# Optimization experiments

Hardware: AMD Instinct MI355X
Metric: run time of the kernel (lower is better)

Reference implementation:

```python
import jax, jax.numpy as jnp
import numpy as np

NUM_USERS = 100000
NUM_ITEMS = 50000
NUM_HIDDEN = 64
NUM_BINS = 10
BATCH = 131072
N_QUAD = 64  # quadrature nodes in incomplete/complete beta
EPS = 1e-6


def _trapz0(y, dt):
    # trapezoidal rule along axis 0 with uniform spacing dt
    return (jnp.sum(y, axis=0) - 0.5 * (y[0] + y[-1])) * dt


def setup_inputs() -> dict:
    key = jax.random.key(0)
    ks = jax.random.split(key, 12)
    return {
        "uid_input": jax.random.randint(ks[0], (BATCH,), 0, NUM_USERS),
        "iid_input": jax.random.randint(ks[1], (BATCH,), 0, NUM_ITEMS),
        "uid_features": 0.1 * jax.random.normal(ks[2], (NUM_USERS, NUM_HIDDEN + 1), jnp.float32),
        "iid_features": 0.1 * jax.random.normal(ks[3], (NUM_ITEMS, NUM_HIDDEN + 1), jnp.float32),
        "uid_bin_terms": 0.1 * jax.random.normal(ks[4], (NUM_USERS, NUM_BINS), jnp.float32),
        "iid_bin_terms": 0.1 * jax.random.normal(ks[5], (NUM_ITEMS, NUM_BINS), jnp.float32),
        "uid_alpha_emb": 0.01 * jax.random.normal(ks[6], (NUM_USERS, 1), jnp.float32),
        "uid_beta_emb": 0.01 * jax.random.normal(ks[7], (NUM_USERS, 1), jnp.float32),
        "iid_alpha_emb": 0.01 * jax.random.normal(ks[8], (NUM_ITEMS, 1), jnp.float32),
        "iid_beta_emb": 0.01 * jax.random.normal(ks[9], (NUM_ITEMS, 1), jnp.float32),
        "global_bias": jnp.asarray(2.0, jnp.float32),
    }


def reference(uid_input, iid_input, uid_features, iid_features,
              uid_bin_terms, iid_bin_terms, uid_alpha_emb, uid_beta_emb,
              iid_alpha_emb, iid_beta_emb, global_bias):
    # embedding lookups (confidence features alias the regular features)
    uf = uid_features[uid_input]          # (B, H+1)
    vf = iid_features[iid_input]          # (B, H+1)
    u = uf[:, :-1]                        # (B, H)
    v = vf[:, :-1]

    # mu / upsilon (upsilon_layer_id == 2: |dot|)
    dot = jnp.sum(u * v, axis=-1, keepdims=True)                    # (B, 1)
    len_prod = (jnp.linalg.norm(u, axis=1, keepdims=True)
                * jnp.linalg.norm(v, axis=1, keepdims=True))
    mu = jnp.clip(0.5 + 0.5 * dot / jnp.maximum(len_prod, EPS), EPS, 1.0 - EPS)
    upsilon = jnp.maximum(jnp.abs(dot), EPS)

    # alpha / beta
    alpha = jnp.maximum(0.01, mu * upsilon)
    beta = jnp.maximum(0.01, upsilon - alpha)
    alpha = global_bias + alpha
    beta = global_bias + beta
    alpha = jnp.maximum(0.01, alpha + uid_alpha_emb[uid_input] + iid_alpha_emb[iid_input])  # (B,1)
    beta = jnp.maximum(0.01, beta + uid_beta_emb[uid_input] + iid_beta_emb[iid_input])      # (B,1)

    # per-pair bin edges via normalized exp + cumsum
    terms = jnp.exp(uid_bin_terms[uid_input] + iid_bin_terms[iid_input])  # (B, NUM_BINS)
    terms = terms / jnp.sum(terms, axis=-1, keepdims=True)
    edges = jnp.cumsum(terms, axis=-1)                                    # (B, NUM_BINS)

    # regularized incomplete beta at interior edges via trapezoidal quadrature
    x = edges[:, :-1]                                  # (B, NB-1)
    t = jnp.linspace(0.0, 1.0, N_QUAD, dtype=alpha.dtype)
    dt = t[1] - t[0]
    t3 = t[:, None, None]                              # (n, 1, 1)
    a3 = alpha[None, :, :]                             # (1, B, 1)
    b3 = beta[None, :, :]
    tx = t3 * x[None]                                  # (n, B, NB-1)
    integrand = (tx ** (a3 - 1.0)) * ((1.0 - tx) ** (b3 - 1.0))
    integrand = integrand * (t3 <= x[None]).astype(integrand.dtype)
    Bx_ab = _trapz0(integrand, dt)                     # (B, NB-1)

    # complete beta B(a, b)
    c_int = (t[None, :] ** (alpha - 1.0)) * ((1.0 - t[None, :]) ** (beta - 1.0))  # (B, n)
    B_ab = (jnp.sum(c_int, axis=-1) - 0.5 * (c_int[:, 0] + c_int[:, -1])) * dt    # (B,)

    cdf = Bx_ab / B_ab[:, None]                        # (B, NB-1)
    cdf = jnp.concatenate([cdf, jnp.ones_like(alpha)], axis=-1)  # (B, NB)
    mass = jnp.concatenate([cdf[:, :1], cdf[:, 1:] - cdf[:, :-1]], axis=-1)
    return mass
```

## Files before the change

### kernel.cpp

```cpp
#include <hip/hip_runtime.h>
#include <math.h>

#define BLOCK 256
#define SPB (BLOCK / 4)

struct F4a4 { float a, b, c, d; };

__device__ __forceinline__ float exp2_fast(float x) {
#if __has_builtin(__builtin_amdgcn_exp2f)
    return __builtin_amdgcn_exp2f(x);
#else
    return __expf(x * 0.69314718055994531f);
#endif
}

__device__ __forceinline__ double exp_f64_fast(double x) {
    const double L2E = 1.4426950408889634074;
    const double LN2 = 0.69314718055994530942;
    double n = rint(x * L2E);
    double r = fma(x, L2E, -n);
    double w = r * LN2;
    double p = 2.08767569878680989792e-9;
    p = fma(p, w, 2.50521083854417187751e-8);
    p = fma(p, w, 2.75573192239858906526e-7);
    p = fma(p, w, 2.75573192239858925110e-6);
    p = fma(p, w, 2.48015873015873015873e-5);
    p = fma(p, w, 1.98412698412698412698e-4);
    p = fma(p, w, 1.38888888888888888889e-3);
    p = fma(p, w, 8.33333333333333333333e-3);
    p = fma(p, w, 4.16666666666666666667e-2);
    p = fma(p, w, 1.66666666666666666667e-1);
    p = fma(p, w, 0.5);
    p = fma(p, w, 1.0);
    p = fma(p, w, 1.0);
    const double sc = __longlong_as_double((long long)(1023 + (int)n) << 52);
    return p * sc;
}

__global__ __launch_bounds__(BLOCK) void lbd_kernel(
    const int* __restrict__ uid_in, const int* __restrict__ iid_in,
    const float* __restrict__ uf,  const float* __restrict__ vf,
    const float* __restrict__ ubt, const float* __restrict__ ibt,
    const float* __restrict__ uae, const float* __restrict__ ube,
    const float* __restrict__ iae, const float* __restrict__ ibe,
    const float* __restrict__ gbp, float* __restrict__ out, int B)
{
    __shared__ float2 s_num[72];
    __shared__ float2 s_den[64];
    const int tid = threadIdx.x;
    if (tid < 72) {
        const double STEP0 = 1.0 / 63.0;
        float tf = (tid >= 63) ? 1.0f : (float)((double)tid * STEP0);
        const float lt = __log2f(tf);
        s_num[tid] = make_float2(tf, lt);
        if (tid < 64) s_den[tid] = make_float2(lt, __log2f(1.0f - tf));
    }
    __syncthreads();

    const int sub = tid & 3;
    const int s0  = blockIdx.x * SPB + (tid >> 2);
    const bool valid = (s0 < B);
    const int s = valid ? s0 : (B - 1);

    const int u = uid_in[s];
    const int v = iid_in[s];

    const float* pu = uf + (long long)u * 65;
    const float* pv = vf + (long long)v * 65;
    float dotp = 0.f, sup = 0.f, svp = 0.f;
#pragma unroll
    for (int c = 0; c < 4; ++c) {
        const F4a4 a = *(const F4a4*)(pu + c * 16 + sub * 4);
        const F4a4 b = *(const F4a4*)(pv + c * 16 + sub * 4);
        dotp += a.a * b.a + a.b * b.b + a.c * b.c + a.d * b.d;
        sup  += a.a * a.a + a.b * a.b + a.c * a.c + a.d * a.d;
        svp  += b.a * b.a + b.b * b.b + b.c * b.c + b.d * b.d;
    }
#pragma unroll
    for (int d = 1; d < 4; d <<= 1) {
        dotp += __shfl_xor(dotp, d, 64);
        sup  += __shfl_xor(sup,  d, 64);
        svp  += __shfl_xor(svp,  d, 64);
    }

    float emb;
    {
        const float* ep = (sub == 0) ? (uae + u)
                        : (sub == 1) ? (iae + v)
                        : (sub == 2) ? (ube + u)
                        :              (ibe + v);
        emb = *ep;
    }
    const float ua_ = __shfl(emb, 0, 4);
    const float ia_ = __shfl(emb, 1, 4);
    const float ub_ = __shfl(emb, 2, 4);
    const float ib_ = __shfl(emb, 3, 4);

    const float gb = gbp[0];
    const float len_prod = sqrtf(sup) * sqrtf(svp);
    const float EPS = 1e-6f;
    const float HI  = (float)(1.0 - 1e-6);
    float mu = 0.5f + (0.5f * dotp) / fmaxf(len_prod, EPS);
    mu = fminf(fmaxf(mu, EPS), HI);
    const float ups = fmaxf(fabsf(dotp), EPS);
    const float al0 = fmaxf(0.01f, mu * ups);
    const float be0 = fmaxf(0.01f, ups - al0);
    const float alpha = fmaxf(0.01f, ((gb + al0) + ua_) + ia_);
    const float beta  = fmaxf(0.01f, ((gb + be0) + ub_) + ib_);
    const float am1 = alpha - 1.0f;
    const float bm1 = beta  - 1.0f;

    const double STEP = 1.0 / 63.0;
    const int lb = 3 * sub;
    double e0, e1 = 0.0, e2 = 0.0;
    {
        const long long ur = (long long)u * 10, vr = (long long)v * 10;
        const int i1 = (lb + 1 <= 9) ? lb + 1 : 9;
        const int i2 = (lb + 2 <= 9) ? lb + 2 : 9;
        e0 = exp_f64_fast((double)ubt[ur + lb] + (double)ibt[vr + lb]);
        const double t1 = exp_f64_fast((double)ubt[ur + i1] + (double)ibt[vr + i1]);
        const double t2 = exp_f64_fast((double)ubt[ur + i2] + (double)ibt[vr + i2]);
        if (lb + 1 <= 9) e1 = t1;
        if (lb + 2 <= 9) e2 = t2;
    }
    const double c0 = e0, c1 = c0 + e1, c2 = c1 + e2;
    double p = c2;
#pragma unroll
    for (int d = 1; d < 4; d <<= 1) {
        const double t = __shfl_up(p, d, 4);
        if (sub >= d) p += t;
    }
    const double ssum = __shfl(p, 3, 4);
    const double rsum = 1.0 / ssum;
    const double ex   = p - c2;
    float xf_own[3] = {0.f, 0.f, 0.f}, lx_own[3] = {0.f, 0.f, 0.f};
    int   im_own[3] = {0, 0, 0};
    const double cg0 = ex + c0, cg1 = ex + c1, cg2 = ex + c2;
#pragma unroll
    for (int r = 0; r < 3; ++r) {
        const double cgr = (r == 0) ? cg0 : (r == 1) ? cg1 : cg2;
        if (lb + r <= 8) {
            const double x = cgr * rsum;
            int k = (int)(x * 63.0);
            k = (k > 62) ? 62 : k;
            const int dec = ((double)k * STEP > x) ? 1 : 0;
            const int inc = ((k < 62) && ((double)(k + 1) * STEP <= x)) ? 1 : 0;
            im_own[r] = k + inc - dec;
            xf_own[r] = (float)x;
            lx_own[r] = __log2f(xf_own[r]);
        }
    }

    float xfj[9], alxj[9];
    int   imj[9], Mw[9];
#pragma unroll
    for (int j = 0; j < 9; ++j) {
        const int src  = j / 3;
        const int slot = j % 3;
        const float xo = (slot == 0) ? xf_own[0] : (slot == 1) ? xf_own[1] : xf_own[2];
        const float lo = (slot == 0) ? lx_own[0] : (slot == 1) ? lx_own[1] : lx_own[2];
        const int   io = (slot == 0) ? im_own[0] : (slot == 1) ? im_own[1] : im_own[2];
        xfj[j]  = __shfl(xo, src, 4);
        alxj[j] = am1 * __shfl(lo, src, 4);
        imj[j]  = __shfl(io, src, 4);
        int mm = imj[j];
        mm = max(mm, __shfl_xor(mm, 4, 64));
        mm = max(mm, __shfl_xor(mm, 8, 64));
        mm = max(mm, __shfl_xor(mm, 16, 64));
        mm = max(mm, __shfl_xor(mm, 32, 64));
        Mw[j] = __builtin_amdgcn_readfirstlane((mm + 3) >> 2);
    }

    float accD = 0.f;
#pragma unroll
    for (int m = 0; m < 16; ++m) {
        const float2 dd = s_den[m * 4 + sub];
        accD += exp2_fast(fmaf(bm1, dd.y, am1 * dd.x));
    }

    const float2 P0 = s_num[sub + 1];
    const float2 P1 = s_num[sub + 5];

    float acc[9];

#define MERGED_LOOP(j1, j2)                                                        \
    {                                                                              \
        const float xA = xfj[j1], aA = alxj[j1];                                   \
        const float xB = xfj[j2], aB = alxj[j2];                                   \
        const int   iA = imj[j1], iB = imj[j2];                                    \
        const int   M  = (Mw[j1] > Mw[j2]) ? Mw[j1] : Mw[j2];          \
        float aA0 = 0.f, aA1 = 0.f, aB0 = 0.f, aB1 = 0.f;                          \
        float2 t0 = P0, t1 = P1;                                                   \
        int m = 0;                                                                 \
        for (; m + 2 <= M; m += 2) {                                               \
            const float2 n0 = s_num[(m + 2) * 4 + sub + 1];                        \
            const float2 n1 = s_num[(m + 3) * 4 + sub + 1];                        \
            const int i0 = m * 4 + sub + 1;                                        \
            const int i1 = i0 + 4;                                                 \
            const float wA0 = fmaf(-t0.x, xA, 1.0f);                               \
            const float wA1 = fmaf(-t1.x, xA, 1.0f);                               \
            const float wB0 = fmaf(-t0.x, xB, 1.0f);                               \
            const float wB1 = fmaf(-t1.x, xB, 1.0f);                               \
            const float eA0 = fmaf(bm1, __log2f(wA0), fmaf(am1, t0.y, aA));        \
            const float eA1 = fmaf(bm1, __log2f(wA1), fmaf(am1, t1.y, aA));        \
            const float eB0 = fmaf(bm1, __log2f(wB0), fmaf(am1, t0.y, aB));        \
            const float eB1 = fmaf(bm1, __log2f(wB1), fmaf(am1, t1.y, aB));        \
            const float yA0 = exp2_fast(eA0), yA1 = exp2_fast(eA1);                \
            const float yB0 = exp2_fast(eB0), yB1 = exp2_fast(eB1);                \
            aA0 += (i0 <= iA) ? yA0 : 0.f;                                         \
            aA1 += (i1 <= iA) ? yA1 : 0.f;                                         \
            aB0 += (i0 <= iB) ? yB0 : 0.f;                                         \
            aB1 += (i1 <= iB) ? yB1 : 0.f;                                         \
            t0 = n0; t1 = n1;                                                      \
        }                                                                          \
        if (m < M) {                                                               \
            const int i0 = m * 4 + sub + 1;                                        \
            const float wA0 = fmaf(-t0.x, xA, 1.0f);                               \
            const float wB0 = fmaf(-t0.x, xB, 1.0f);                               \
            const float eA0 = fmaf(bm1, __log2f(wA0), fmaf(am1, t0.y, aA));        \
            const float eB0 = fmaf(bm1, __log2f(wB0), fmaf(am1, t0.y, aB));        \
            aA0 += (i0 <= iA) ? exp2_fast(eA0) : 0.f;                              \
            aB0 += (i0 <= iB) ? exp2_fast(eB0) : 0.f;                              \
        }                                                                          \
        acc[j1] = aA0 + aA1;                                                       \
        acc[j2] = aB0 + aB1;                                                       \
    }

    MERGED_LOOP(0, 1)
    MERGED_LOOP(2, 3)
    MERGED_LOOP(4, 5)
    MERGED_LOOP(6, 7)
#undef MERGED_LOOP

    {
        const float xj  = xfj[8];
        const float axj = alxj[8];
        const int   imv = imj[8];
        const int   M   = Mw[8];
        float a0 = 0.f, a1 = 0.f;
        float2 t0 = P0, t1 = P1;
        int m = 0;
        for (; m + 2 <= M; m += 2) {
            const float2 n0 = s_num[(m + 2) * 4 + sub + 1];
            const float2 n1 = s_num[(m + 3) * 4 + sub + 1];
            const int i0 = m * 4 + sub + 1;
            const int i1 = i0 + 4;
            const float w0 = fmaf(-t0.x, xj, 1.0f);
            const float w1 = fmaf(-t1.x, xj, 1.0f);
            const float e0v = fmaf(bm1, __log2f(w0), fmaf(am1, t0.y, axj));
            const float e1v = fmaf(bm1, __log2f(w1), fmaf(am1, t1.y, axj));
            const float y0 = exp2_fast(e0v);
            const float y1 = exp2_fast(e1v);
            a0 += (i0 <= imv) ? y0 : 0.f;
            a1 += (i1 <= imv) ? y1 : 0.f;
            t0 = n0; t1 = n1;
        }
        if (m < M) {
            const int i0 = m * 4 + sub + 1;
            const float w0 = fmaf(-t0.x, xj, 1.0f);
            const float e0v = fmaf(bm1, __log2f(w0), fmaf(am1, t0.y, axj));
            a0 += (i0 <= imv) ? exp2_fast(e0v) : 0.f;
        }
        acc[8] = a0 + a1;
    }

#pragma unroll
    for (int d = 1; d < 4; d <<= 1) {
        accD += __shfl_xor(accD, d, 64);
#pragma unroll
        for (int j = 0; j < 9; ++j) acc[j] += __shfl_xor(acc[j], d, 64);
    }

    const float dtf = (float)(1.0 / 63.0);
    const float rB  = 1.0f / (accD * dtf);
    float cdfv[9];
#pragma unroll
    for (int j = 0; j < 9; ++j) cdfv[j] = (acc[j] * dtf) * rB;

    const float o0 = (sub == 0) ? cdfv[0]
                   : (sub == 1) ? (cdfv[1] - cdfv[0])
                   : (sub == 2) ? (cdfv[2] - cdfv[1])
                   :              (cdfv[3] - cdfv[2]);
    const float o1 = (sub == 0) ? (cdfv[4] - cdfv[3])
                   : (sub == 1) ? (cdfv[5] - cdfv[4])
                   : (sub == 2) ? (cdfv[6] - cdfv[5])
                   :              (cdfv[7] - cdfv[6]);
    const float o2 = (sub == 0) ? (cdfv[8] - cdfv[7])
                   :              (1.0f - cdfv[8]);
    if (valid) {
        const long long ob = (long long)s * 10;
        out[ob + sub]     = o0;
        out[ob + 4 + sub] = o1;
        if (sub < 2) out[ob + 8 + sub] = o2;
    }
}

extern "C" void kernel_launch(void* const* d_in, const int* in_sizes, int n_in,
                              void* d_out, int out_size, void* d_ws, size_t ws_size,
                              hipStream_t stream) {
    (void)n_in; (void)out_size; (void)d_ws; (void)ws_size;
    const int*   uid = (const int*)d_in[0];
    const int*   iid = (const int*)d_in[1];
    const float* uf  = (const float*)d_in[2];
    const float* vf  = (const float*)d_in[3];
    const float* ubt = (const float*)d_in[4];
    const float* ibt = (const float*)d_in[5];
    const float* uae = (const float*)d_in[6];
    const float* ube = (const float*)d_in[7];
    const float* iae = (const float*)d_in[8];
    const float* ibe = (const float*)d_in[9];
    const float* gb  = (const float*)d_in[10];
    float* out = (float*)d_out;
    const int B = in_sizes[0];
    const int grid = (B + SPB - 1) / SPB;
    hipLaunchKernelGGL(lbd_kernel, dim3(grid), dim3(BLOCK), 0, stream,
                       uid, iid, uf, vf, ubt, ibt, uae, ube, iae, ibe, gb, out, B);
}
```

Baseline: 124.3 us.

## Stage per-sample edge values in LDS and fuse complete-beta sum into last loop

Per-sample edge values (x, log2 x, index bound) are now written to shared memory and read back by every lane of the group, replacing the register shuffle redistribution. The per-pair wave-max bound is computed inside each pair loop. The complete-beta denominator accumulation is merged into the final edge's quadrature loop, which now runs the full 16 iterations instead of a data-dependent bound. The aim is fewer cross-lane shuffles and better interleaving of transcendental work, at the cost of extra LDS traffic, a block barrier, and always running the full range for the last edge.

```diff
diff --git a/kernel.cpp b/kernel.cpp
--- a/kernel.cpp
+++ b/kernel.cpp
@@ -45,20 +45,34 @@
     const float* __restrict__ iae, const float* __restrict__ ibe,
     const float* __restrict__ gbp, float* __restrict__ out, int B)
 {
-    __shared__ float2 s_num[72];
-    __shared__ float2 s_den[64];
+    __shared__ float2 s_num[76];
+    __shared__ float2 s_den[72];
+    __shared__ float  s_x [SPB][10];
+    __shared__ float  s_lx[SPB][10];
+    __shared__ int    s_im[SPB][10];
+
     const int tid = threadIdx.x;
-    if (tid < 72) {
+    {
         const double STEP0 = 1.0 / 63.0;
-        float tf = (tid >= 63) ? 1.0f : (float)((double)tid * STEP0);
-        const float lt = __log2f(tf);
-        s_num[tid] = make_float2(tf, lt);
-        if (tid < 64) s_den[tid] = make_float2(lt, __log2f(1.0f - tf));
+        if (tid < 76) {
+            const float tf = (tid >= 63) ? 1.0f : (float)((double)tid * STEP0);
+            s_num[tid] = make_float2(tf, __log2f(tf));
+        }
+        if (tid < 72) {
+            float l1 = 0.f, l2 = 0.f;
+            if (tid < 64) {
+                const float tf = (tid >= 63) ? 1.0f : (float)((double)tid * STEP0);
+                l1 = __log2f(tf);
+                l2 = __log2f(1.0f - tf);
+            }
+            s_den[tid] = make_float2(l1, l2);
+        }
     }
     __syncthreads();
 
     const int sub = tid & 3;
-    const int s0  = blockIdx.x * SPB + (tid >> 2);
+    const int g   = tid >> 2;
+    const int s0  = blockIdx.x * SPB + g;
     const bool valid = (s0 < B);
     const int s = valid ? s0 : (B - 1);
 
@@ -133,8 +147,6 @@
     const double ssum = __shfl(p, 3, 4);
     const double rsum = 1.0 / ssum;
     const double ex   = p - c2;
-    float xf_own[3] = {0.f, 0.f, 0.f}, lx_own[3] = {0.f, 0.f, 0.f};
-    int   im_own[3] = {0, 0, 0};
     const double cg0 = ex + c0, cg1 = ex + c1, cg2 = ex + c2;
 #pragma unroll
     for (int r = 0; r < 3; ++r) {
@@ -145,50 +157,31 @@
             k = (k > 62) ? 62 : k;
             const int dec = ((double)k * STEP > x) ? 1 : 0;
             const int inc = ((k < 62) && ((double)(k + 1) * STEP <= x)) ? 1 : 0;
-            im_own[r] = k + inc - dec;
-            xf_own[r] = (float)x;
-            lx_own[r] = __log2f(xf_own[r]);
+            const float xf = (float)x;
+            s_im[g][lb + r] = k + inc - dec;
+            s_x [g][lb + r] = xf;
+            s_lx[g][lb + r] = __log2f(xf);
         }
     }
-
-    float xfj[9], alxj[9];
-    int   imj[9], Mw[9];
-#pragma unroll
-    for (int j = 0; j < 9; ++j) {
-        const int src  = j / 3;
-        const int slot = j % 3;
-        const float xo = (slot == 0) ? xf_own[0] : (slot == 1) ? xf_own[1] : xf_own[2];
-        const float lo = (slot == 0) ? lx_own[0] : (slot == 1) ? lx_own[1] : lx_own[2];
-        const int   io = (slot == 0) ? im_own[0] : (slot == 1) ? im_own[1] : im_own[2];
-        xfj[j]  = __shfl(xo, src, 4);
-        alxj[j] = am1 * __shfl(lo, src, 4);
-        imj[j]  = __shfl(io, src, 4);
-        int mm = imj[j];
-        mm = max(mm, __shfl_xor(mm, 4, 64));
-        mm = max(mm, __shfl_xor(mm, 8, 64));
-        mm = max(mm, __shfl_xor(mm, 16, 64));
-        mm = max(mm, __shfl_xor(mm, 32, 64));
-        Mw[j] = __builtin_amdgcn_readfirstlane((mm + 3) >> 2);
-    }
-
-    float accD = 0.f;
-#pragma unroll
-    for (int m = 0; m < 16; ++m) {
-        const float2 dd = s_den[m * 4 + sub];
-        accD += exp2_fast(fmaf(bm1, dd.y, am1 * dd.x));
-    }
+    __syncthreads();
 
     const float2 P0 = s_num[sub + 1];
     const float2 P1 = s_num[sub + 5];
 
     float acc[9];
-
-#define MERGED_LOOP(j1, j2)                                                        \
+    float accD = 0.f;
+
+#define PAIR_LOOP(j1, j2)                                                          \
     {                                                                              \
-        const float xA = xfj[j1], aA = alxj[j1];                                   \
-        const float xB = xfj[j2], aB = alxj[j2];                                   \
-        const int   iA = imj[j1], iB = imj[j2];                                    \
-        const int   M  = (Mw[j1] > Mw[j2]) ? Mw[j1] : Mw[j2];          \
+        const float xA = s_x[g][j1],          xB = s_x[g][j2];                     \
+        const float aA = am1 * s_lx[g][j1],   aB = am1 * s_lx[g][j2];              \
+        const int   iA = s_im[g][j1],         iB = s_im[g][j2];                    \
+        int mm = (iA > iB) ? iA : iB;                                              \
+        mm = max(mm, __shfl_xor(mm, 4, 64));    \
+        mm = max(mm, __shfl_xor(mm, 8, 64));                                       \
+        mm = max(mm, __shfl_xor(mm, 16, 64));                                      \
+        mm = max(mm, __shfl_xor(mm, 32, 64));                                      \
+        const int M = __builtin_amdgcn_readfirstlane((mm + 3) >> 2);               \
         float aA0 = 0.f, aA1 = 0.f, aB0 = 0.f, aB1 = 0.f;                          \
         float2 t0 = P0, t1 = P1;                                                   \
         int m = 0;                                                                 \
@@ -226,23 +219,25 @@
         acc[j2] = aB0 + aB1;                                                       \
     }
 
-    MERGED_LOOP(0, 1)
-    MERGED_LOOP(2, 3)
-    MERGED_LOOP(4, 5)
-    MERGED_LOOP(6, 7)
-#undef MERGED_LOOP
+    PAIR_LOOP(0, 1)
+    PAIR_LOOP(2, 3)
+    PAIR_LOOP(4, 5)
+    PAIR_LOOP(6, 7)
+#undef PAIR_LOOP
 
     {
-        const float xj  = xfj[8];
-        const float axj = alxj[8];
-        const int   imv = imj[8];
-        const int   M   = Mw[8];
+        const float xj  = s_x[g][8];
+        const float axj = am1 * s_lx[g][8];
+        const int   imv = s_im[g][8];
         float a0 = 0.f, a1 = 0.f;
         float2 t0 = P0, t1 = P1;
-        int m = 0;
-        for (; m + 2 <= M; m += 2) {
-            const float2 n0 = s_num[(m + 2) * 4 + sub + 1];
-            const float2 n1 = s_num[(m + 3) * 4 + sub + 1];
+        float2 d0 = s_den[sub], d1 = s_den[sub + 4];
+#pragma unroll 4
+        for (int m = 0; m + 2 <= 16; m += 2) {
+            const float2 n0  = s_num[(m + 2) * 4 + sub + 1];
+            const float2 n1  = s_num[(m + 3) * 4 + sub + 1];
+            const float2 nd0 = s_den[(m + 2) * 4 + sub];
+            const float2 nd1 = s_den[(m + 3) * 4 + sub];
             const int i0 = m * 4 + sub + 1;
             const int i1 = i0 + 4;
             const float w0 = fmaf(-t0.x, xj, 1.0f);
@@ -253,13 +248,9 @@
             const float y1 = exp2_fast(e1v);
             a0 += (i0 <= imv) ? y0 : 0.f;
             a1 += (i1 <= imv) ? y1 : 0.f;
-            t0 = n0; t1 = n1;
-        }
-        if (m < M) {
-            const int i0 = m * 4 + sub + 1;
-            const float w0 = fmaf(-t0.x, xj, 1.0f);
-            const float e0v = fmaf(bm1, __log2f(w0), fmaf(am1, t0.y, axj));
-            a0 += (i0 <= imv) ? exp2_fast(e0v) : 0.f;
+            accD += exp2_fast(fmaf(bm1, d0.y, am1 * d0.x));
+            accD += exp2_fast(fmaf(bm1, d1.y, am1 * d1.x));
+            t0 = n0; t1 = n1; d0 = nd0; d1 = nd1;
         }
         acc[8] = a0 + a1;
     }
```

Result: no change. 122.8 us (-1.3%).
